# Kernel optimization log

Hardware: AMD Instinct MI355X
Metric: run time of the kernel (lower is better)

## Reference

```python
import jax, jax.numpy as jnp
import numpy as np

B = 262144          # batch
D = 128             # in_dim == out_dim
BS = 16             # block size
K = 8               # number of blocks
RANK = 4            # low-rank blocks' rank
DENSE = np.array([0, 3, 6])   # block ids with mode 'dense'
DIAG = np.array([1, 4, 7])    # block ids with mode 'diagonal'
LR = np.array([2, 5])         # block ids with mode 'lowrank'
EPS = 1e-8


def setup_inputs() -> dict:
    key = jax.random.key(0)
    k1, k2, k3, k4, k5 = jax.random.split(key, 5)
    x = jax.random.normal(k1, (B, D), dtype=jnp.float32)
    # dense blocks: torch init is identity (d_in==d_out); add noise so math is non-trivial
    W_dense = jnp.eye(BS, dtype=jnp.float32)[None] + 0.1 * jax.random.normal(k2, (len(DENSE), BS, BS), dtype=jnp.float32)
    # diagonal blocks: torch init is ones; perturb slightly
    s_diag = 1.0 + 0.1 * jax.random.normal(k3, (len(DIAG), BS), dtype=jnp.float32)
    # lowrank blocks: xavier-uniform-like scale
    lim = float(np.sqrt(6.0 / (BS + RANK)))
    U = jax.random.uniform(k4, (len(LR), BS, RANK), dtype=jnp.float32, minval=-lim, maxval=lim)
    V = jax.random.uniform(k5, (len(LR), BS, RANK), dtype=jnp.float32, minval=-lim, maxval=lim)
    return {"x": x, "W_dense": W_dense, "s_diag": s_diag, "U": U, "V": V}


def reference(x, W_dense, s_diag, U, V):
    # blocks are contiguous [16*j, 16*(j+1)), so gather == reshape to [B, K, BS]
    x3 = x.reshape(B, K, BS)
    # dense blocks: torch Linear y = x @ W.T, W is [d_out, d_in]
    yd = jnp.einsum('bkd,kod->bko', x3[:, DENSE], W_dense)
    # diagonal blocks: elementwise scale
    yg = x3[:, DIAG] * s_diag
    # lowrank blocks: x @ V @ U.T
    yl = jnp.einsum('bkr,kor->bko', jnp.einsum('bkd,kdr->bkr', x3[:, LR], V), U)
    y = jnp.zeros_like(x3).at[:, DENSE].set(yd).at[:, DIAG].set(yg).at[:, LR].set(yl)
    y = y.reshape(B, D)
    # l2 normalize (normalize=True)
    norm = jnp.linalg.norm(y, axis=-1, keepdims=True)
    return y / (norm + EPS)
```

## Files before the change

kernel.cpp:

```cpp
#include <hip/hip_runtime.h>

#define BATCH   262144
#define DDIM    128
#define GRID    2048
#define NITER   8

template <int CTRL>
__device__ __forceinline__ float fdpp(float v) {
    int i = __builtin_bit_cast(int, v);
    i = __builtin_amdgcn_mov_dpp(i, CTRL, 0xF, 0xF, true);
    return __builtin_bit_cast(float, i);
}
__device__ __forceinline__ float fswz16(float v) {
    int i = __builtin_bit_cast(int, v);
    i = __builtin_amdgcn_ds_swizzle(i, 0x401F);
    return __builtin_bit_cast(float, i);
}

__global__ __launch_bounds__(256, 3) void bdla_kernel(
    const float* __restrict__ x,
    const float* __restrict__ Wd,
    const float* __restrict__ sd,
    const float* __restrict__ U,
    const float* __restrict__ V,
    float* __restrict__ out)
{
    __shared__ float lds[1072];
    const int tid = threadIdx.x;
    for (int i = tid; i < 768; i += 256) lds[i] = Wd[i];
    if (tid < 48)  lds[768 + tid] = sd[tid];
    if (tid < 128) lds[816 + tid] = U[tid];
    if (tid < 128) lds[944 + tid] = V[tid];
    __syncthreads();

    const int lane   = tid & 63;
    const int lane32 = lane & 31;
    const int half   = lane >> 5;
    const int j      = lane32 >> 2;
    const int sub    = lane32 & 3;
    const int mode   = j % 3;
    const int k      = j / 3;

    float A[4][16];
    if (mode == 0) {
        const float* w = &lds[k * 256];
#pragma unroll
        for (int oo = 0; oo < 4; ++oo) {
            const int o = sub * 4 + oo;
#pragma unroll
            for (int m = 0; m < 4; ++m)
#pragma unroll
                for (int c = 0; c < 4; ++c)
                    A[oo][m * 4 + c] = w[o * 16 + ((sub ^ m) * 4 + c)];
        }
    } else if (mode == 1) {
        const float* s = &lds[768 + k * 16];
#pragma unroll
        for (int oo = 0; oo < 4; ++oo)
#pragma unroll
            for (int m = 0; m < 4; ++m)
#pragma unroll
                for (int c = 0; c < 4; ++c)
                    A[oo][m * 4 + c] = (m == 0 && c == oo) ? s[sub * 4 + oo] : 0.0f;
    } else {
        const float* u = &lds[816 + k * 64];
        const float* v = &lds[944 + k * 64];
#pragma unroll
        for (int oo = 0; oo < 4; ++oo) {
            const int o = sub * 4 + oo;
#pragma unroll
            for (int m = 0; m < 4; ++m)
#pragma unroll
                for (int c = 0; c < 4; ++c) {
                    const int d = (sub ^ m) * 4 + c;
                    float acc = 0.0f;
#pragma unroll
                    for (int r = 0; r < 4; ++r)
                        acc += u[o * 4 + r] * v[d * 4 + r];
                    A[oo][m * 4 + c] = acc;
                }
        }
    }

#pragma unroll
    for (int oo = 0; oo < 4; ++oo)
#pragma unroll
        for (int t = 0; t < 16; ++t)
            asm volatile("" : "+v"(A[oo][t]));

    const int gw = blockIdx.x * 4 + (tid >> 6);
    const float* xbase = x   + (size_t)(gw * 4 + half) * DDIM + lane32 * 4;
    float*       obase = out + (size_t)(gw * 4 + half) * DDIM + lane32 * 4;
    const size_t istep = (size_t)(GRID * 4 * 4) * DDIM;

    float4 a0 = *(const float4*)(xbase);
    float4 b0 = *(const float4*)(xbase + 2 * DDIM);
    float4 a1 = *(const float4*)(xbase + istep);
    float4 b1 = *(const float4*)(xbase + istep + 2 * DDIM);

#pragma unroll
    for (int it = 0; it < NITER; ++it) {
        float4 a2, b2;
        if (it + 2 < NITER) {
            a2 = *(const float4*)(xbase + (size_t)(it + 2) * istep);
            b2 = *(const float4*)(xbase + (size_t)(it + 2) * istep + 2 * DDIM);
        }

        float ga[16], gb[16];
        ga[0] = a0.x; ga[1] = a0.y; ga[2] = a0.z; ga[3] = a0.w;
        gb[0] = b0.x; gb[1] = b0.y; gb[2] = b0.z; gb[3] = b0.w;
        ga[4]  = fdpp<0xB1>(a0.x); ga[5]  = fdpp<0xB1>(a0.y);
        ga[6]  = fdpp<0xB1>(a0.z); ga[7]  = fdpp<0xB1>(a0.w);
        gb[4]  = fdpp<0xB1>(b0.x); gb[5]  = fdpp<0xB1>(b0.y);
        gb[6]  = fdpp<0xB1>(b0.z); gb[7]  = fdpp<0xB1>(b0.w);
        ga[8]  = fdpp<0x4E>(a0.x); ga[9]  = fdpp<0x4E>(a0.y);
        ga[10] = fdpp<0x4E>(a0.z); ga[11] = fdpp<0x4E>(a0.w);
        gb[8]  = fdpp<0x4E>(b0.x); gb[9]  = fdpp<0x4E>(b0.y);
        gb[10] = fdpp<0x4E>(b0.z); gb[11] = fdpp<0x4E>(b0.w);
        ga[12] = fdpp<0x1B>(a0.x); ga[13] = fdpp<0x1B>(a0.y);
        ga[14] = fdpp<0x1B>(a0.z); ga[15] = fdpp<0x1B>(a0.w);
        gb[12] = fdpp<0x1B>(b0.x); gb[13] = fdpp<0x1B>(b0.y);
        gb[14] = fdpp<0x1B>(b0.z); gb[15] = fdpp<0x1B>(b0.w);

        float ya0 = 0.f, ya1 = 0.f, ya2 = 0.f, ya3 = 0.f;
        float yb0 = 0.f, yb1 = 0.f, yb2 = 0.f, yb3 = 0.f;
#pragma unroll
        for (int t = 0; t < 16; ++t) {
            ya0 = fmaf(A[0][t], ga[t], ya0);
            ya1 = fmaf(A[1][t], ga[t], ya1);
            ya2 = fmaf(A[2][t], ga[t], ya2);
            ya3 = fmaf(A[3][t], ga[t], ya3);
            yb0 = fmaf(A[0][t], gb[t], yb0);
            yb1 = fmaf(A[1][t], gb[t], yb1);
            yb2 = fmaf(A[2][t], gb[t], yb2);
            yb3 = fmaf(A[3][t], gb[t], yb3);
        }

        float ssa = ya0 * ya0 + ya1 * ya1 + ya2 * ya2 + ya3 * ya3;
        float ssb = yb0 * yb0 + yb1 * yb1 + yb2 * yb2 + yb3 * yb3;
        ssa += fdpp<0xB1>(ssa);  ssb += fdpp<0xB1>(ssb);
        ssa += fdpp<0x4E>(ssa);  ssb += fdpp<0x4E>(ssb);
        ssa += fdpp<0x141>(ssa); ssb += fdpp<0x141>(ssb);
        ssa += fdpp<0x140>(ssa); ssb += fdpp<0x140>(ssb);
        ssa += fswz16(ssa);      ssb += fswz16(ssb);
        const float inva = 1.0f / (sqrtf(ssa) + 1e-8f);
        const float invb = 1.0f / (sqrtf(ssb) + 1e-8f);

        float4 yva, yvb;
        yva.x = ya0 * inva; yva.y = ya1 * inva; yva.z = ya2 * inva; yva.w = ya3 * inva;
        yvb.x = yb0 * invb; yvb.y = yb1 * invb; yvb.z = yb2 * invb; yvb.w = yb3 * invb;
        *(float4*)(obase + (size_t)it * istep)            = yva;
        *(float4*)(obase + (size_t)it * istep + 2 * DDIM) = yvb;

        a0 = a1; b0 = b1; a1 = a2; b1 = b2;
    }
}

extern "C" void kernel_launch(void* const* d_in, const int* in_sizes, int n_in,
                              void* d_out, int out_size, void* d_ws, size_t ws_size,
                              hipStream_t stream) {
    const float* x  = (const float*)d_in[0];
    const float* Wd = (const float*)d_in[1];
    const float* sd = (const float*)d_in[2];
    const float* U  = (const float*)d_in[3];
    const float* V  = (const float*)d_in[4];
    float* out = (float*)d_out;
    (void)in_sizes; (void)n_in; (void)out_size; (void)d_ws; (void)ws_size;

    dim3 grid(GRID), block(256);
    hipLaunchKernelGGL(bdla_kernel, grid, block, 0, stream, x, Wd, sd, U, V, out);
}
```

Baseline: 243.4 us.

## Stage x rows through LDS with async global_load_lds double buffering

Replaces the register-prefetch loop with a scheme where each block loads 16-row chunks of x directly into double-buffered LDS using global_load_lds, and lanes read their block segment from LDS. Each lane now owns two output columns instead of four, which halves the resident weight registers, and the launch bound is raised to allow more waves per SIMD. The aim is more latency hiding and occupancy for this bandwidth-bound kernel. It adds LDS traffic, a cross-half shuffle in the norm reduction, and narrower float2 stores. The manual vmcnt waits also run without a barrier between waves; this is safe only because each wave loads and then reads its own rows.

```diff
diff --git a/kernel.cpp b/kernel.cpp
--- a/kernel.cpp
+++ b/kernel.cpp
@@ -3,7 +3,9 @@
 #define BATCH   262144
 #define DDIM    128
 #define GRID    2048
-#define NITER   8
+#define ROWS_PER_BLOCK 128
+#define CHUNK   16
+#define NCHUNK  8
 
 template <int CTRL>
 __device__ __forceinline__ float fdpp(float v) {
@@ -16,8 +18,14 @@
     i = __builtin_amdgcn_ds_swizzle(i, 0x401F);
     return __builtin_bit_cast(float, i);
 }
+__device__ __forceinline__ void gload_lds16(const float* g, float* l) {
+    __builtin_amdgcn_global_load_lds(
+        (const __attribute__((address_space(1))) void*)g,
+        (__attribute__((address_space(3))) void*)l,
+        16, 0, 0);
+}
 
-__global__ __launch_bounds__(256, 3) void bdla_kernel(
+__global__ __launch_bounds__(256, 6) void bdla_kernel(
     const float* __restrict__ x,
     const float* __restrict__ Wd,
     const float* __restrict__ sd,
@@ -25,134 +33,141 @@
     const float* __restrict__ V,
     float* __restrict__ out)
 {
-    __shared__ float lds[1072];
-    const int tid = threadIdx.x;
-    for (int i = tid; i < 768; i += 256) lds[i] = Wd[i];
-    if (tid < 48)  lds[768 + tid] = sd[tid];
-    if (tid < 128) lds[816 + tid] = U[tid];
-    if (tid < 128) lds[944 + tid] = V[tid];
+    __shared__ float wlds[1072];
+    __shared__ float xbuf[2][CHUNK * DDIM];
+
+    const int tid  = threadIdx.x;
+    const int lane = tid & 63;
+    const int w    = tid >> 6;
+    const int j    = lane >> 3;
+    const int rot  = j >> 1;
+    const int o0   = 2 * (lane & 7);
+    const int o1   = o0 + 1;
+
+    for (int i = tid; i < 768; i += 256) wlds[i] = Wd[i];
+    if (tid < 48)  wlds[768 + tid] = sd[tid];
+    if (tid < 128) wlds[816 + tid] = U[tid];
+    if (tid < 128) wlds[944 + tid] = V[tid];
+
+    const size_t blockrow = (size_t)blockIdx.x * ROWS_PER_BLOCK;
+
+    {
+        const float* gs = x + (blockrow + w * 4) * DDIM;
+        float* ls = &xbuf[0][w * 4 * DDIM];
+        gload_lds16(gs + lane * 4,       ls + lane * 4);
+        gload_lds16(gs + 256 + lane * 4, ls + 256 + lane * 4);
+    }
+
     __syncthreads();
 
-    const int lane   = tid & 63;
-    const int lane32 = lane & 31;
-    const int half   = lane >> 5;
-    const int j      = lane32 >> 2;
-    const int sub    = lane32 & 3;
-    const int mode   = j % 3;
-    const int k      = j / 3;
-
-    float A[4][16];
-    if (mode == 0) {
-        const float* w = &lds[k * 256];
+    float B0[16], B1[16];
+    {
+        const int mode = j % 3, k = j / 3;
+        if (mode == 0) {
+            const float* wm = &wlds[k * 256];
 #pragma unroll
-        for (int oo = 0; oo < 4; ++oo) {
-            const int o = sub * 4 + oo;
+            for (int cc = 0; cc < 4; ++cc) {
+                const int ce = (cc + rot) & 3;
 #pragma unroll
-            for (int m = 0; m < 4; ++m)
+                for (int e = 0; e < 4; ++e) {
+                    B0[cc * 4 + e] = wm[o0 * 16 + ce * 4 + e];
+                    B1[cc * 4 + e] = wm[o1 * 16 + ce * 4 + e];
+                }
+            }
+        } else if (mode == 1) {
+            const float* s = &wlds[768 + k * 16];
 #pragma unroll
-                for (int c = 0; c < 4; ++c)
-                    A[oo][m * 4 + c] = w[o * 16 + ((sub ^ m) * 4 + c)];
-        }
-    } else if (mode == 1) {
-        const float* s = &lds[768 + k * 16];
+            for (int cc = 0; cc < 4; ++cc) {
+                const int ce = (cc + rot) & 3;
 #pragma unroll
-        for (int oo = 0; oo < 4; ++oo)
+                for (int e = 0; e < 4; ++e) {
+                    const int d = ce * 4 + e;
+                    B0[cc * 4 + e] = (d == o0) ? s[o0] : 0.0f;
+                    B1[cc * 4 + e] = (d == o1) ? s[o1] : 0.0f;
+                }
+            }
+        } else {
+            const float* u = &wlds[816 + k * 64];
+            const float* v = &wlds[944 + k * 64];
 #pragma unroll
-            for (int m = 0; m < 4; ++m)
+            for (int cc = 0; cc < 4; ++cc) {
+                const int ce = (cc + rot) & 3;
 #pragma unroll
-                for (int c = 0; c < 4; ++c)
-                    A[oo][m * 4 + c] = (m == 0 && c == oo) ? s[sub * 4 + oo] : 0.0f;
-    } else {
-        const float* u = &lds[816 + k * 64];
-        const float* v = &lds[944 + k * 64];
+                for (int e = 0; e < 4; ++e) {
+                    const int d = ce * 4 + e;
+                    float a0 = 0.f, a1 = 0.f;
 #pragma unroll
-        for (int oo = 0; oo < 4; ++oo) {
-            const int o = sub * 4 + oo;
-#pragma unroll
-            for (int m = 0; m < 4; ++m)
-#pragma unroll
-                for (int c = 0; c < 4; ++c) {
-                    const int d = (sub ^ m) * 4 + c;
-                    float acc = 0.0f;
-#pragma unroll
-                    for (int r = 0; r < 4; ++r)
-                        acc += u[o * 4 + r] * v[d * 4 + r];
-                    A[oo][m * 4 + c] = acc;
+                    for (int r = 0; r < 4; ++r) {
+                        a0 += u[o0 * 4 + r] * v[d * 4 + r];
+                        a1 += u[o1 * 4 + r] * v[d * 4 + r];
+                    }
+                    B0[cc * 4 + e] = a0;
+                    B1[cc * 4 + e] = a1;
                 }
+            }
         }
     }
+#pragma unroll
+    for (int t = 0; t < 16; ++t) asm volatile("" : "+v"(B0[t]), "+v"(B1[t]));
 
 #pragma unroll
-    for (int oo = 0; oo < 4; ++oo)
+    for (int c = 0; c < NCHUNK; ++c) {
+        if (c + 1 < NCHUNK) {
+            const float* gs = x + (blockrow + (size_t)(c + 1) * CHUNK + w * 4) * DDIM;
+            float* ls = &xbuf[(c + 1) & 1][w * 4 * DDIM];
+            gload_lds16(gs + lane * 4,       ls + lane * 4);
+            gload_lds16(gs + 256 + lane * 4, ls + 256 + lane * 4);
+        }
+        if (c + 1 < NCHUNK) asm volatile("s_waitcnt vmcnt(2)" ::: "memory");
+        else                asm volatile("s_waitcnt vmcnt(0)" ::: "memory");
+
+        const float* xb = &xbuf[c & 1][0];
 #pragma unroll
-        for (int t = 0; t < 16; ++t)
-            asm volatile("" : "+v"(A[oo][t]));
+        for (int pr = 0; pr < 2; ++pr) {
+            const int r0 = w * 4 + pr * 2;
+            const int r1 = r0 + 1;
+            float y0a = 0.f, y1a = 0.f, y0b = 0.f, y1b = 0.f;
+#pragma unroll
+            for (int cc = 0; cc < 4; ++cc) {
+                const int ce = (cc + rot) & 3;
+                const float4 xa = *(const float4*)&xb[r0 * DDIM + j * 16 + ce * 4];
+                const float4 xv = *(const float4*)&xb[r1 * DDIM + j * 16 + ce * 4];
+                y0a = fmaf(B0[cc * 4 + 0], xa.x, y0a);
+                y1a = fmaf(B1[cc * 4 + 0], xa.x, y1a);
+                y0b = fmaf(B0[cc * 4 + 0], xv.x, y0b);
+                y1b = fmaf(B1[cc * 4 + 0], xv.x, y1b);
+                y0a = fmaf(B0[cc * 4 + 1], xa.y, y0a);
+                y1a = fmaf(B1[cc * 4 + 1], xa.y, y1a);
+                y0b = fmaf(B0[cc * 4 + 1], xv.y, y0b);
+                y1b = fmaf(B1[cc * 4 + 1], xv.y, y1b);
+                y0a = fmaf(B0[cc * 4 + 2], xa.z, y0a);
+                y1a = fmaf(B1[cc * 4 + 2], xa.z, y1a);
+                y0b = fmaf(B0[cc * 4 + 2], xv.z, y0b);
+                y1b = fmaf(B1[cc * 4 + 2], xv.z, y1b);
+                y0a = fmaf(B0[cc * 4 + 3], xa.w, y0a);
+                y1a = fmaf(B1[cc * 4 + 3], xa.w, y1a);
+                y0b = fmaf(B0[cc * 4 + 3], xv.w, y0b);
+                y1b = fmaf(B1[cc * 4 + 3], xv.w, y1b);
+            }
 
-    const int gw = blockIdx.x * 4 + (tid >> 6);
-    const float* xbase = x   + (size_t)(gw * 4 + half) * DDIM + lane32 * 4;
-    float*       obase = out + (size_t)(gw * 4 + half) * DDIM + lane32 * 4;
-    const size_t istep = (size_t)(GRID * 4 * 4) * DDIM;
+            float ssa = y0a * y0a + y1a * y1a;
+            float ssb = y0b * y0b + y1b * y1b;
+            ssa += fdpp<0xB1>(ssa);  ssb += fdpp<0xB1>(ssb);
+            ssa += fdpp<0x4E>(ssa);  ssb += fdpp<0x4E>(ssb);
+            ssa += fdpp<0x141>(ssa); ssb += fdpp<0x141>(ssb);
+            ssa += fdpp<0x140>(ssa); ssb += fdpp<0x140>(ssb);
+            ssa += fswz16(ssa);      ssb += fswz16(ssb);
+            ssa += __shfl_xor(ssa, 32); ssb += __shfl_xor(ssb, 32);
+            const float inva = 1.0f / (sqrtf(ssa) + 1e-8f);
+            const float invb = 1.0f / (sqrtf(ssb) + 1e-8f);
 
-    float4 a0 = *(const float4*)(xbase);
-    float4 b0 = *(const float4*)(xbase + 2 * DDIM);
-    float4 a1 = *(const float4*)(xbase + istep);
-    float4 b1 = *(const float4*)(xbase + istep + 2 * DDIM);
-
-#pragma unroll
-    for (int it = 0; it < NITER; ++it) {
-        float4 a2, b2;
-        if (it + 2 < NITER) {
-            a2 = *(const float4*)(xbase + (size_t)(it + 2) * istep);
-            b2 = *(const float4*)(xbase + (size_t)(it + 2) * istep + 2 * DDIM);
+            float* po = out + (blockrow + (size_t)c * CHUNK + r0) * DDIM + 2 * lane;
+            float2 oa, ob;
+            oa.x = y0a * inva; oa.y = y1a * inva;
+            ob.x = y0b * invb; ob.y = y1b * invb;
+            *(float2*)po          = oa;
+            *(float2*)(po + DDIM) = ob;
         }
-
-        float ga[16], gb[16];
-        ga[0] = a0.x; ga[1] = a0.y; ga[2] = a0.z; ga[3] = a0.w;
-        gb[0] = b0.x; gb[1] = b0.y; gb[2] = b0.z; gb[3] = b0.w;
-        ga[4]  = fdpp<0xB1>(a0.x); ga[5]  = fdpp<0xB1>(a0.y);
-        ga[6]  = fdpp<0xB1>(a0.z); ga[7]  = fdpp<0xB1>(a0.w);
-        gb[4]  = fdpp<0xB1>(b0.x); gb[5]  = fdpp<0xB1>(b0.y);
-        gb[6]  = fdpp<0xB1>(b0.z); gb[7]  = fdpp<0xB1>(b0.w);
-        ga[8]  = fdpp<0x4E>(a0.x); ga[9]  = fdpp<0x4E>(a0.y);
-        ga[10] = fdpp<0x4E>(a0.z); ga[11] = fdpp<0x4E>(a0.w);
-        gb[8]  = fdpp<0x4E>(b0.x); gb[9]  = fdpp<0x4E>(b0.y);
-        gb[10] = fdpp<0x4E>(b0.z); gb[11] = fdpp<0x4E>(b0.w);
-        ga[12] = fdpp<0x1B>(a0.x); ga[13] = fdpp<0x1B>(a0.y);
-        ga[14] = fdpp<0x1B>(a0.z); ga[15] = fdpp<0x1B>(a0.w);
-        gb[12] = fdpp<0x1B>(b0.x); gb[13] = fdpp<0x1B>(b0.y);
-        gb[14] = fdpp<0x1B>(b0.z); gb[15] = fdpp<0x1B>(b0.w);
-
-        float ya0 = 0.f, ya1 = 0.f, ya2 = 0.f, ya3 = 0.f;
-        float yb0 = 0.f, yb1 = 0.f, yb2 = 0.f, yb3 = 0.f;
-#pragma unroll
-        for (int t = 0; t < 16; ++t) {
-            ya0 = fmaf(A[0][t], ga[t], ya0);
-            ya1 = fmaf(A[1][t], ga[t], ya1);
-            ya2 = fmaf(A[2][t], ga[t], ya2);
-            ya3 = fmaf(A[3][t], ga[t], ya3);
-            yb0 = fmaf(A[0][t], gb[t], yb0);
-            yb1 = fmaf(A[1][t], gb[t], yb1);
-            yb2 = fmaf(A[2][t], gb[t], yb2);
-            yb3 = fmaf(A[3][t], gb[t], yb3);
-        }
-
-        float ssa = ya0 * ya0 + ya1 * ya1 + ya2 * ya2 + ya3 * ya3;
-        float ssb = yb0 * yb0 + yb1 * yb1 + yb2 * yb2 + yb3 * yb3;
-        ssa += fdpp<0xB1>(ssa);  ssb += fdpp<0xB1>(ssb);
-        ssa += fdpp<0x4E>(ssa);  ssb += fdpp<0x4E>(ssb);
-        ssa += fdpp<0x141>(ssa); ssb += fdpp<0x141>(ssb);
-        ssa += fdpp<0x140>(ssa); ssb += fdpp<0x140>(ssb);
-        ssa += fswz16(ssa);      ssb += fswz16(ssb);
-        const float inva = 1.0f / (sqrtf(ssa) + 1e-8f);
-        const float invb = 1.0f / (sqrtf(ssb) + 1e-8f);
-
-        float4 yva, yvb;
-        yva.x = ya0 * inva; yva.y = ya1 * inva; yva.z = ya2 * inva; yva.w = ya3 * inva;
-        yvb.x = yb0 * invb; yvb.y = yb1 * invb; yvb.z = yb2 * invb; yvb.w = yb3 * invb;
-        *(float4*)(obase + (size_t)it * istep)            = yva;
-        *(float4*)(obase + (size_t)it * istep + 2 * DDIM) = yvb;
-
-        a0 = a1; b0 = b1; a1 = a2; b1 = b2;
     }
 }
 
```

Result: no change. 245.3 us (+0.8%).
